# Kernel tuning notes

Measured on AMD Instinct MI355X. Metric: run time of the kernel, lower is better.

## Reference

```python
import jax, jax.numpy as jnp
import numpy as np
import math

B, S, D = 2, 2048, 1024
H, KV, HD = 16, 4, 64
G = H // KV          # kv groups
CAP = 50.0           # attention soft-cap
EPS = 1e-6           # RMSNorm eps


def _rmsnorm(x, w):
    return x * jax.lax.rsqrt(jnp.mean(x * x, axis=-1, keepdims=True) + EPS) * w


def _rope(x, freqs):
    # x: (b, h, s, hd); freqs: (S, hd//2, 2) with [...,0]=cos, [...,1]=sin
    s = x.shape[2]
    xp = x.reshape(*x.shape[:-1], -1, 2)
    cos = freqs[:s, :, 0][None, None]   # (1,1,s,hd//2)
    sin = freqs[:s, :, 1][None, None]
    x0, x1 = xp[..., 0], xp[..., 1]
    out = jnp.stack([x0 * cos - x1 * sin, x0 * sin + x1 * cos], axis=-1)
    return out.reshape(x.shape)


def setup_inputs() -> dict:
    key = jax.random.key(0)
    ks = jax.random.split(key, 6)
    x = jax.random.normal(ks[0], (B, S, D), dtype=jnp.float32)
    # realistic RoPE table: theta_i = pos / 10000^(2i/hd)
    inv_freq = 1.0 / (10000.0 ** (np.arange(0, HD, 2, dtype=np.float32) / HD))
    theta = np.arange(S, dtype=np.float32)[:, None] * inv_freq[None, :]
    rope_freqs = jnp.asarray(np.stack([np.cos(theta), np.sin(theta)], axis=-1))
    sc = 0.02
    wq = jax.random.normal(ks[1], (2 * H * HD, D), dtype=jnp.float32) * sc
    wk = jax.random.normal(ks[2], (2 * KV * HD, D), dtype=jnp.float32) * sc
    wv = jax.random.normal(ks[3], (KV * HD, D), dtype=jnp.float32) * sc
    wo = jax.random.normal(ks[4], (D, H * HD), dtype=jnp.float32) * sc
    q_norm_w = jnp.ones((HD,), dtype=jnp.float32)
    k_norm_w = jnp.ones((HD,), dtype=jnp.float32)
    diff_lambda = jnp.array([0.8], dtype=jnp.float32)
    return {"x": x, "rope_freqs": rope_freqs, "wq": wq, "wk": wk, "wv": wv,
            "wo": wo, "q_norm_w": q_norm_w, "k_norm_w": k_norm_w,
            "diff_lambda": diff_lambda}


def reference(x, rope_freqs, wq, wk, wv, wo, q_norm_w, k_norm_w, diff_lambda):
    b, s, _ = x.shape
    # projections (torch Linear: y = x @ W^T)
    q = (x @ wq.T).reshape(b, s, H, 2 * HD).transpose(0, 2, 1, 3)   # (b,H,s,2hd)
    k = (x @ wk.T).reshape(b, s, KV, 2 * HD).transpose(0, 2, 1, 3)  # (b,KV,s,2hd)
    v = (x @ wv.T).reshape(b, s, KV, HD).transpose(0, 2, 1, 3)      # (b,KV,s,hd)
    q1, q2 = jnp.split(q, 2, axis=-1)
    k1, k2 = jnp.split(k, 2, axis=-1)
    # QK-norm (before RoPE, as in the torch module)
    q1, q2 = _rmsnorm(q1, q_norm_w), _rmsnorm(q2, q_norm_w)
    k1, k2 = _rmsnorm(k1, k_norm_w), _rmsnorm(k2, k_norm_w)
    # RoPE
    q1, q2 = _rope(q1, rope_freqs), _rope(q2, rope_freqs)
    k1, k2 = _rope(k1, rope_freqs), _rope(k2, rope_freqs)
    # GQA expansion: each kv head repeated G times contiguously
    k1 = jnp.repeat(k1, G, axis=1)
    k2 = jnp.repeat(k2, G, axis=1)
    v = jnp.repeat(v, G, axis=1)
    scale = 1.0 / math.sqrt(HD)
    scores1 = jnp.einsum('bhqd,bhkd->bhqk', q1, k1) * scale
    scores2 = jnp.einsum('bhqd,bhkd->bhqk', q2, k2) * scale
    # soft-cap
    scores1 = CAP * jnp.tanh(scores1 / CAP)
    scores2 = CAP * jnp.tanh(scores2 / CAP)
    mask = jnp.triu(jnp.full((s, s), -jnp.inf, dtype=scores1.dtype), 1)
    attn1 = jax.nn.softmax(scores1 + mask, axis=-1)
    attn2 = jax.nn.softmax(scores2 + mask, axis=-1)
    diff_attn = attn1 - diff_lambda[0] * attn2
    out = jnp.einsum('bhqk,bhkd->bhqd', diff_attn, v)
    out = out.transpose(0, 2, 1, 3).reshape(b, s, H * HD)
    return out @ wo.T
```

## Files before the change

### kernel.cpp

```cpp
#include <hip/hip_runtime.h>
#include <hip/hip_bf16.h>

#define B_ 2
#define S_ 2048
#define D_ 1024
#define H_ 16
#define KV_ 4
#define HD_ 64
#define G_ (H_ / KV_)
#define NCAT 2816
#define VOFF 2560

typedef __attribute__((ext_vector_type(8))) short short8;
typedef __attribute__((ext_vector_type(4))) short short4v;
typedef __attribute__((ext_vector_type(2))) int int2v;
typedef __attribute__((ext_vector_type(4))) float floatx4;

using gvoid_p = const __attribute__((address_space(1))) void*;
using lvoid_p = __attribute__((address_space(3))) void*;

__device__ inline void gload_lds16(const short* g, short* l) {
    __builtin_amdgcn_global_load_lds((gvoid_p)(const void*)g, (lvoid_p)(void*)l, 16, 0, 0);
}

__device__ inline int cvt_pk_bf16(float lo, float hi) {
    int r;
    asm volatile("v_cvt_pk_bf16_f32 %0, %1, %2" : "=v"(r) : "v"(lo), "v"(hi));
    return r;
}

__global__ void cvt5_kernel(const float* s0, const float* s1, const float* s2,
                            const float* s3, const float* s4,
                            __hip_bfloat16* d0, __hip_bfloat16* d1, __hip_bfloat16* d2,
                            __hip_bfloat16* d3, __hip_bfloat16* d4,
                            int n0, int n1, int n2, int n3, int n4) {
    const float* s; __hip_bfloat16* d; int n;
    switch (blockIdx.y) {
        case 0: s = s0; d = d0; n = n0; break;
        case 1: s = s1; d = d1; n = n1; break;
        case 2: s = s2; d = d2; n = n2; break;
        case 3: s = s3; d = d3; n = n3; break;
        default: s = s4; d = d4; n = n4; break;
    }
    int nv = n >> 2;
    for (int i = blockIdx.x * blockDim.x + threadIdx.x; i < nv;
         i += gridDim.x * blockDim.x) {
        floatx4 v = ((const floatx4*)s)[i];
        short4v o;
#pragma unroll
        for (int e = 0; e < 4; ++e) {
            __hip_bfloat16 hh = __float2bfloat16(v[e]);
            o[e] = __builtin_bit_cast(short, hh);
        }
        ((short4v*)d)[i] = o;
    }
}

template <typename OutT>
__global__ __launch_bounds__(256) void gemm_bt_lds(const short* __restrict__ A,
                                                   const short* __restrict__ Bm,
                                                   OutT* __restrict__ C,
                                                   int M, int N, int K) {
    __shared__ __align__(16) short As[2][128 * 32];
    __shared__ __align__(16) short Bs[2][128 * 32];
    int tid = threadIdx.x;
    int wid = tid >> 6, lane = tid & 63;
    int wr = wid >> 1, wc = wid & 1;
    int r = lane & 15, kq = lane >> 4;

    int nwg = gridDim.x * gridDim.y;
    int orig = blockIdx.y * gridDim.x + blockIdx.x;
    int wg = (orig & 7) * (nwg >> 3) + (orig >> 3);
    int bx = wg % gridDim.x, by = wg / gridDim.x;

    long m0 = (long)by * 128;
    long n0 = (long)bx * 128;

    const short* gA0 = A + (m0 + (tid >> 2)) * (long)K + (tid & 3) * 8;
    const short* gA1 = A + (m0 + 64 + (tid >> 2)) * (long)K + (tid & 3) * 8;
    const short* gB0 = Bm + (n0 + (tid >> 2)) * (long)K + (tid & 3) * 8;
    const short* gB1 = Bm + (n0 + 64 + (tid >> 2)) * (long)K + (tid & 3) * 8;

    auto stage = [&](int buf, int k0) {
        gload_lds16(gA0 + k0, &As[buf][wid * 512]);
        gload_lds16(gA1 + k0, &As[buf][2048 + wid * 512]);
        gload_lds16(gB0 + k0, &Bs[buf][wid * 512]);
        gload_lds16(gB1 + k0, &Bs[buf][2048 + wid * 512]);
    };

    floatx4 acc[4][4];
#pragma unroll
    for (int i = 0; i < 4; ++i)
#pragma unroll
        for (int j = 0; j < 4; ++j) acc[i][j] = {0.f, 0.f, 0.f, 0.f};

    int nt = K >> 5;
    stage(0, 0);
    for (int t = 0; t < nt; ++t) {
        int cur = t & 1;
        __builtin_amdgcn_s_barrier();
        if (t + 1 < nt) {
            stage(cur ^ 1, (t + 1) << 5);
            asm volatile("s_waitcnt vmcnt(4)" ::: "memory");
        } else {
            asm volatile("s_waitcnt vmcnt(0)" ::: "memory");
        }
        __builtin_amdgcn_sched_barrier(0);
        __builtin_amdgcn_s_barrier();
        short8 a[4], b[4];
#pragma unroll
        for (int mi = 0; mi < 4; ++mi)
            a[mi] = *(const short8*)&As[cur][(wr * 64 + mi * 16 + r) * 32 + kq * 8];
#pragma unroll
        for (int ni = 0; ni < 4; ++ni)
            b[ni] = *(const short8*)&Bs[cur][(wc * 64 + ni * 16 + r) * 32 + kq * 8];
#pragma unroll
        for (int mi = 0; mi < 4; ++mi)
#pragma unroll
            for (int ni = 0; ni < 4; ++ni)
                acc[mi][ni] = __builtin_amdgcn_mfma_f32_16x16x32_bf16(
                    a[mi], b[ni], acc[mi][ni], 0, 0, 0);
    }
    int col_l = lane & 15, row_l = (lane >> 4) * 4;
#pragma unroll
    for (int mi = 0; mi < 4; ++mi)
#pragma unroll
        for (int ni = 0; ni < 4; ++ni) {
            long col = n0 + wc * 64 + ni * 16 + col_l;
            long row0 = m0 + wr * 64 + mi * 16 + row_l;
#pragma unroll
            for (int j = 0; j < 4; ++j) {
                float v = acc[mi][ni][j];
                if constexpr (__is_same(OutT, float))
                    C[(row0 + j) * N + col] = v;
                else
                    C[(row0 + j) * N + col] = __float2bfloat16(v);
            }
        }
}

__global__ void norm_rope_kernel(const __hip_bfloat16* __restrict__ buf,
                                 __hip_bfloat16* __restrict__ outb,
                                 const float* __restrict__ freqs,
                                 const float* __restrict__ w, int nvec, int nh,
                                 int tstride, int colbase) {
    int gt = blockIdx.x * blockDim.x + threadIdx.x;
    int gw = gt >> 6;
    int lane = gt & 63;
    if (gw >= nvec) return;
    int t = gw / (nh * 2);
    int rem = gw - t * (nh * 2);
    int s = t & (S_ - 1);
    const __hip_bfloat16* v = buf + (long)t * tstride + colbase + rem * 64;
    float x = __bfloat162float(v[lane]);
    float ss = x * x;
#pragma unroll
    for (int off = 32; off; off >>= 1) ss += __shfl_xor(ss, off);
    float r = rsqrtf(ss * (1.f / 64.f) + 1e-6f);
    x = x * r * w[lane];
    int i = lane >> 1;
    float c  = freqs[(s * (HD_ / 2) + i) * 2];
    float sn = freqs[(s * (HD_ / 2) + i) * 2 + 1];
    float p = __shfl_xor(x, 1);
    float y = (lane & 1) ? fmaf(p, sn, x * c) : fmaf(x, c, -(p * sn));
    outb[(long)gw * 64 + lane] = __float2bfloat16(y);
}

__global__ __launch_bounds__(256) void v_transpose_kernel(const short* __restrict__ src,
                                                          short* __restrict__ dst) {
    __shared__ short ls[64][72];
    int s0 = blockIdx.x * 64;
    int kv = blockIdx.y, b = blockIdx.z;
    int tid = threadIdx.x;
    const short* base = src + ((long)(b * S_ + s0)) * NCAT + VOFF + kv * 64;
    {
        int rr = tid >> 2, cc = (tid & 3) * 16;
        *(short8*)&ls[rr][cc]     = *(const short8*)(base + (long)rr * NCAT + cc);
        *(short8*)&ls[rr][cc + 8] = *(const short8*)(base + (long)rr * NCAT + cc + 8);
    }
    __syncthreads();
    short* ob = dst + ((long)(b * KV_ + kv) * 64) * S_ + s0;
    {
        int d = tid >> 2, sl = (tid & 3) * 16;
        short8 o0, o1;
#pragma unroll
        for (int e = 0; e < 8; ++e) { o0[e] = ls[sl + e][d]; o1[e] = ls[sl + 8 + e][d]; }
        *(short8*)(ob + (long)d * S_ + sl)     = o0;
        *(short8*)(ob + (long)d * S_ + sl + 8) = o1;
    }
}

__global__ __launch_bounds__(256, 4) void attn_kernel(const short* __restrict__ qb,
                                                      const short* __restrict__ kbuf,
                                                      const short* __restrict__ vtb,
                                                      __hip_bfloat16* __restrict__ ob,
                                                      float* __restrict__ part,
                                                      float* __restrict__ lpart,
                                                      const float* __restrict__ lam_p) {
    __shared__ __align__(16) short Ks[2][32][128];
    __shared__ __align__(16) short Vt[2][64][40];

    int tid = threadIdx.x, w = tid >> 6, lane = tid & 63;
    int b = blockIdx.z, h = blockIdx.y, kv = h / G_;
    int p = (int)blockIdx.x >> 1, e = (int)blockIdx.x & 1;
    int qtA = p, qtB = 31 - p;
    int r = lane & 15, kq = lane >> 4;
    float lam = lam_p[0];

    floatx4 acc[2][4];
    floatx4 accl[2];
    short8 qa[2][2];

    const short* vbase = vtb + (long)(b * KV_ + kv) * 64 * S_;
    const float c1 = 0.18033688f, nc4 = -3.7570e-7f, zoff = -17.3123405f;
    const short one_bf = (short)0x3F80;
    short4v ones4 = {one_bf, one_bf, one_bf, one_bf};

    int ch1 = tid + 256;
    int krow0 = tid >> 4, kcs0 = ((tid & 15) ^ (krow0 & 7)) * 8;
    int krow1 = ch1 >> 4, kcs1 = ((ch1 & 15) ^ (krow1 & 7)) * 8;
    const short* kgb = kbuf + ((long)b * S_ * KV_ + kv) * 128;
    int vd = tid >> 2, vch = tid & 3;

    auto issueK = [&](int buf, int ki) {
        long rb = (long)(ki * 32) * (KV_ * 128);
        gload_lds16(kgb + rb + (long)krow0 * (KV_ * 128) + kcs0, &Ks[buf][0][0] + w * 512);
        gload_lds16(kgb + rb + (long)krow1 * (KV_ * 128) + kcs1, &Ks[buf][0][0] + 2048 + w * 512);
    };
    auto loadV = [&](int kb) {
        return *(const short8*)(vbase + (long)vd * S_ + kb + vch * 8);
    };

    auto reset_acc = [&]() {
#pragma unroll
        for (int m = 0; m < 2; ++m) {
            accl[m] = {0.f, 0.f, 0.f, 0.f};
#pragma unroll
            for (int dt = 0; dt < 4; ++dt) acc[m][dt] = {0.f, 0.f, 0.f, 0.f};
        }
    };
    auto load_q = [&](int q0) {
        const short* qrow = qb + ((long)(b * S_ + q0 + r) * H_ + h) * 128;
        qa[0][0] = *(const short8*)(qrow + kq * 8);
        qa[0][1] = *(const short8*)(qrow + 32 + kq * 8);
        qa[1][0] = *(const short8*)(qrow + 64 + kq * 8);
        qa[1][1] = *(const short8*)(qrow + 96 + kq * 8);
    };

    auto tile_compute = [&](int cur, int kb, int q0, bool domask) {
        int rel = q0 + r - kb;
#pragma unroll
        for (int m = 0; m < 2; ++m) {
            floatx4 sacc[2];
#pragma unroll
            for (int nt = 0; nt < 2; ++nt) {
                sacc[nt] = {0.f, 0.f, 0.f, 0.f};
                const short* row = &Ks[cur][nt * 16 + r][0];
                short8 a0 = *(const short8*)(row + (((m * 8) + kq) ^ (r & 7)) * 8);
                short8 a1 = *(const short8*)(row + (((m * 8) + 4 + kq) ^ (r & 7)) * 8);
                sacc[nt] = __builtin_amdgcn_mfma_f32_16x16x32_bf16(a0, qa[m][0], sacc[nt], 0, 0, 0);
                sacc[nt] = __builtin_amdgcn_mfma_f32_16x16x32_bf16(a1, qa[m][1], sacc[nt], 0, 0, 0);
            }
            short4v pa[2];
#pragma unroll
            for (int nt = 0; nt < 2; ++nt) {
                float pv[4];
#pragma unroll
                for (int j = 0; j < 4; ++j) {
                    float raw = sacc[nt][j];
                    float r2 = raw * raw;
                    float z = fmaf(raw, fmaf(r2, nc4, c1), zoff);
                    pv[j] = __builtin_amdgcn_exp2f(z);
                    if (domask && (nt * 16 + kq * 4 + j > rel)) pv[j] = 0.f;
                }
                int lo = cvt_pk_bf16(pv[0], pv[1]);
                int hi = cvt_pk_bf16(pv[2], pv[3]);
                pa[nt] = __builtin_bit_cast(short4v, int2v{lo, hi});
            }
#pragma unroll
            for (int dt = 0; dt < 4; ++dt) {
#pragma unroll
                for (int nt = 0; nt < 2; ++nt) {
                    short4v vb = *(const short4v*)&Vt[cur][dt * 16 + r][nt * 16 + kq * 4];
                    acc[m][dt] = __builtin_amdgcn_mfma_f32_16x16x16bf16_1k(
                        pa[nt], vb, acc[m][dt], 0, 0, 0);
                }
            }
#pragma unroll
            for (int nt = 0; nt < 2; ++nt)
                accl[m] = __builtin_amdgcn_mfma_f32_16x16x16bf16_1k(
                    pa[nt], ones4, accl[m], 0, 0, 0);
        }
    };

    auto run = [&](int qt, int ki0, int ki1, bool diag) {
        int q0 = qt * 64 + w * 16;
        load_q(q0);
        reset_acc();
        int nseg = ki1 - ki0;
        issueK(0, ki0);
        short8 rva = loadV(ki0 * 32), rvb;
        for (int ii = 0; ii < nseg; ++ii) {
            int ki = ki0 + ii, cur = ii & 1;
            bool pre = (ii + 1 < nseg);
            if (pre) issueK(cur ^ 1, ki + 1);
            if (pre) asm volatile("s_waitcnt vmcnt(2)" ::: "memory");
            else     asm volatile("s_waitcnt vmcnt(0)" ::: "memory");
            __builtin_amdgcn_sched_barrier(0);
            if (cur == 0) {
                *(short8*)&Vt[0][vd][vch * 8] = rva;
                if (pre) rvb = loadV((ki + 1) * 32);
            } else {
                *(short8*)&Vt[1][vd][vch * 8] = rvb;
                if (pre) rva = loadV((ki + 1) * 32);
            }
            asm volatile("s_waitcnt lgkmcnt(0)" ::: "memory");
            __builtin_amdgcn_sched_barrier(0);
            __builtin_amdgcn_s_barrier();
            tile_compute(cur, ki * 32, q0, diag && ((ki >> 1) == qt));
        }
        __builtin_amdgcn_s_barrier();
    };

    if (e == 0) {
        run(qtA, 0, 2 * qtA + 2, true);
        {
            int q0 = qtA * 64 + w * 16;
#pragma unroll
            for (int j = 0; j < 4; ++j) {
                float i1 = 1.f / accl[0][j];
                float i2 = lam / accl[1][j];
                int qr = q0 + kq * 4 + j;
                __hip_bfloat16* orow = ob + ((long)(b * S_ + qr) * H_ + h) * 64;
#pragma unroll
                for (int dt = 0; dt < 4; ++dt) {
                    float val = acc[0][dt][j] * i1 - acc[1][dt][j] * i2;
                    orow[dt * 16 + r] = __float2bfloat16(val);
                }
            }
        }
        run(qtB, 0, 31 - 2 * p, false);
    } else {
        run(qtB, 31 - 2 * p, 64 - 2 * p, true);
    }

    {
        long slot = (long)(b * H_ + h) * 16 + (qtB - 16);
        long base = ((slot * 2 + e) * 2) * 4096L;
        int qloc = w * 16 + kq * 4;
#pragma unroll
        for (int m = 0; m < 2; ++m)
#pragma unroll
            for (int dt = 0; dt < 4; ++dt)
#pragma unroll
                for (int j = 0; j < 4; ++j)
                    part[base + m * 4096L + (qloc + j) * 64 + dt * 16 + r] = acc[m][dt][j];
        if (r == 0) {
#pragma unroll
            for (int m = 0; m < 2; ++m)
#pragma unroll
                for (int j = 0; j < 4; ++j)
                    lpart[((slot * 2 + e) * 2 + m) * 64 + qloc + j] = accl[m][j];
        }
    }
}

__global__ __launch_bounds__(256) void attn_merge_kernel(const float* __restrict__ part,
                                                         const float* __restrict__ lpart,
                                                         __hip_bfloat16* __restrict__ ob,
                                                         const float* __restrict__ lam_p) {
    long sid = blockIdx.x;
    int t16 = sid & 15;
    int h = (sid >> 4) & (H_ - 1);
    int b = (int)(sid >> 8);
    int qt = 16 + t16;
    float lam = lam_p[0];
    const float* p0 = part + sid * 4 * 4096L;
    const float* p1 = part + (sid * 4 + 2) * 4096L;
    const float* l0 = lpart + sid * 4 * 64L;
    const float* l1 = lpart + (sid * 4 + 2) * 64L;
    int tid = threadIdx.x;
#pragma unroll
    for (int i = 0; i < 16; ++i) {
        int idx = i * 256 + tid;
        int q = idx >> 6, d = idx & 63;
        float a1 = p0[q * 64 + d] + p1[q * 64 + d];
        float a2 = p0[4096 + q * 64 + d] + p1[4096 + q * 64 + d];
        float L1 = l0[q] + l1[q];
        float L2 = l0[64 + q] + l1[64 + q];
        float val = a1 / L1 - lam * (a2 / L2);
        ob[((long)(b * S_ + qt * 64 + q) * H_ + h) * 64 + d] = __float2bfloat16(val);
    }
}

extern "C" void kernel_launch(void* const* d_in, const int* in_sizes, int n_in,
                              void* d_out, int out_size, void* d_ws, size_t ws_size,
                              hipStream_t stream) {
    const float* x     = (const float*)d_in[0];
    const float* freqs = (const float*)d_in[1];
    const float* wq    = (const float*)d_in[2];
    const float* wk    = (const float*)d_in[3];
    const float* wv    = (const float*)d_in[4];
    const float* wo    = (const float*)d_in[5];
    const float* qnw   = (const float*)d_in[6];
    const float* knw   = (const float*)d_in[7];
    const float* lam   = (const float*)d_in[8];
    float* out = (float*)d_out;

    const int T = B_ * S_;
    char* ws = (char*)d_ws;
    size_t off = 0;
    auto alloc = [&](size_t bytes) {
        void* p = ws + off;
        off += (bytes + 255) & ~(size_t)255;
        return p;
    };
    __hip_bfloat16* xb   = (__hip_bfloat16*)alloc((size_t)T * D_ * 2);
    __hip_bfloat16* wcat = (__hip_bfloat16*)alloc((size_t)NCAT * D_ * 2);
    __hip_bfloat16* wob  = (__hip_bfloat16*)alloc((size_t)D_ * D_ * 2);
    __hip_bfloat16* qkvb = (__hip_bfloat16*)alloc((size_t)T * NCAT * 2);
    __hip_bfloat16* qb16 = (__hip_bfloat16*)alloc((size_t)T * 2 * H_ * HD_ * 2);
    __hip_bfloat16* kb16 = (__hip_bfloat16*)alloc((size_t)T * 2 * KV_ * HD_ * 2);
    __hip_bfloat16* vT   = (__hip_bfloat16*)alloc((size_t)B_ * KV_ * HD_ * S_ * 2);
    float* part  = (float*)alloc((size_t)512 * 2 * 2 * 4096 * 4);
    float* lpart = (float*)alloc((size_t)512 * 2 * 2 * 64 * 4);
    __hip_bfloat16* aob  = xb;

    cvt5_kernel<<<dim3(2048, 5), 256, 0, stream>>>(
        x, wq, wk, wv, wo,
        xb, wcat, wcat + (size_t)2 * H_ * HD_ * D_,
        wcat + (size_t)(2 * H_ * HD_ + 2 * KV_ * HD_) * D_, wob,
        T * D_, 2 * H_ * HD_ * D_, 2 * KV_ * HD_ * D_, KV_ * HD_ * D_, D_ * D_);

    gemm_bt_lds<__hip_bfloat16><<<dim3(NCAT / 128, T / 128), 256, 0, stream>>>(
        (const short*)xb, (const short*)wcat, qkvb, T, NCAT, D_);

    {
        int nvq = T * H_ * 2;
        norm_rope_kernel<<<(nvq * 64 + 255) / 256, 256, 0, stream>>>(
            qkvb, qb16, freqs, qnw, nvq, H_, NCAT, 0);
        int nvk = T * KV_ * 2;
        norm_rope_kernel<<<(nvk * 64 + 255) / 256, 256, 0, stream>>>(
            qkvb, kb16, freqs, knw, nvk, KV_, NCAT, 2 * H_ * HD_);
        v_transpose_kernel<<<dim3(S_ / 64, KV_, B_), 256, 0, stream>>>(
            (const short*)qkvb, (short*)vT);
    }

    attn_kernel<<<dim3(32, H_, B_), 256, 0, stream>>>(
        (const short*)qb16, (const short*)kb16, (const short*)vT, aob, part, lpart, lam);
    attn_merge_kernel<<<512, 256, 0, stream>>>(part, lpart, aob, lam);

    gemm_bt_lds<float><<<dim3(D_ / 128, T / 128), 256, 0, stream>>>(
        (const short*)aob, (const short*)wob, out, T, D_, D_);
}
```

Measured before the change: 174.1 us.

## Use 16x16x32 MFMA for PV, preload V fragments, triple-buffer K tiles

The P·V product and the row-sum accumulation now use 16x16x32 bf16 MFMAs. Both key sub-tiles are packed into one short8 operand, which halves the number of PV and row-sum MFMA instructions. V fragments are loaded from LDS once per tile, before the two head-half loops, instead of inside each loop. K shared memory goes from two buffers to three, rotating so the prefetch writes a buffer that no lagging wave can still be reading. The extra buffer raises LDS use per block, which could reduce occupancy, and the PV operand layout has to stay consistent with the k-index mapping of the larger MFMA.

```diff
diff --git a/kernel.cpp b/kernel.cpp
--- a/kernel.cpp
+++ b/kernel.cpp
@@ -14,6 +14,7 @@
 typedef __attribute__((ext_vector_type(8))) short short8;
 typedef __attribute__((ext_vector_type(4))) short short4v;
 typedef __attribute__((ext_vector_type(2))) int int2v;
+typedef __attribute__((ext_vector_type(4))) int int4v;
 typedef __attribute__((ext_vector_type(4))) float floatx4;
 
 using gvoid_p = const __attribute__((address_space(1))) void*;
@@ -197,7 +198,7 @@
                                                       float* __restrict__ part,
                                                       float* __restrict__ lpart,
                                                       const float* __restrict__ lam_p) {
-    __shared__ __align__(16) short Ks[2][32][128];
+    __shared__ __align__(16) short Ks[3][32][128];
     __shared__ __align__(16) short Vt[2][64][40];
 
     int tid = threadIdx.x, w = tid >> 6, lane = tid & 63;
@@ -214,7 +215,7 @@
     const short* vbase = vtb + (long)(b * KV_ + kv) * 64 * S_;
     const float c1 = 0.18033688f, nc4 = -3.7570e-7f, zoff = -17.3123405f;
     const short one_bf = (short)0x3F80;
-    short4v ones4 = {one_bf, one_bf, one_bf, one_bf};
+    short8 ones8 = {one_bf, one_bf, one_bf, one_bf, one_bf, one_bf, one_bf, one_bf};
 
     int ch1 = tid + 256;
     int krow0 = tid >> 4, kcs0 = ((tid & 15) ^ (krow0 & 7)) * 8;
@@ -247,49 +248,55 @@
         qa[1][1] = *(const short8*)(qrow + 96 + kq * 8);
     };
 
-    auto tile_compute = [&](int cur, int kb, int q0, bool domask) {
+    auto tile_compute = [&](int bk, int cv, int kb, int q0, bool domask) {
         int rel = q0 + r - kb;
+        short8 vb[4];
+#pragma unroll
+        for (int dt = 0; dt < 4; ++dt) {
+            const short* vrow = &Vt[cv][dt * 16 + r][0];
+            int2v lo = *(const int2v*)(vrow + 4 * kq);
+            int2v hi = *(const int2v*)(vrow + 16 + 4 * kq);
+            vb[dt] = __builtin_bit_cast(short8, int4v{lo[0], lo[1], hi[0], hi[1]});
+        }
 #pragma unroll
         for (int m = 0; m < 2; ++m) {
             floatx4 sacc[2];
 #pragma unroll
             for (int nt = 0; nt < 2; ++nt) {
                 sacc[nt] = {0.f, 0.f, 0.f, 0.f};
-                const short* row = &Ks[cur][nt * 16 + r][0];
+                const short* row = &Ks[bk][nt * 16 + r][0];
                 short8 a0 = *(const short8*)(row + (((m * 8) + kq) ^ (r & 7)) * 8);
                 short8 a1 = *(const short8*)(row + (((m * 8) + 4 + kq) ^ (r & 7)) * 8);
                 sacc[nt] = __builtin_amdgcn_mfma_f32_16x16x32_bf16(a0, qa[m][0], sacc[nt], 0, 0, 0);
                 sacc[nt] = __builtin_amdgcn_mfma_f32_16x16x32_bf16(a1, qa[m][1], sacc[nt], 0, 0, 0);
             }
-            short4v pa[2];
-#pragma unroll
-            for (int nt = 0; nt < 2; ++nt) {
-                float pv[4];
+            float pv[2][4];
+#pragma unroll
+            for (int nt = 0; nt < 2; ++nt)
 #pragma unroll
                 for (int j = 0; j < 4; ++j) {
                     float raw = sacc[nt][j];
                     float r2 = raw * raw;
                     float z = fmaf(raw, fmaf(r2, nc4, c1), zoff);
-                    pv[j] = __builtin_amdgcn_exp2f(z);
-                    if (domask && (nt * 16 + kq * 4 + j > rel)) pv[j] = 0.f;
+                    pv[nt][j] = __builtin_amdgcn_exp2f(z);
                 }
-                int lo = cvt_pk_bf16(pv[0], pv[1]);
-                int hi = cvt_pk_bf16(pv[2], pv[3]);
-                pa[nt] = __builtin_bit_cast(short4v, int2v{lo, hi});
+            if (domask) {
+#pragma unroll
+                for (int nt = 0; nt < 2; ++nt)
+#pragma unroll
+                    for (int j = 0; j < 4; ++j)
+                        if (nt * 16 + kq * 4 + j > rel) pv[nt][j] = 0.f;
             }
-#pragma unroll
-            for (int dt = 0; dt < 4; ++dt) {
-#pragma unroll
-                for (int nt = 0; nt < 2; ++nt) {
-                    short4v vb = *(const short4v*)&Vt[cur][dt * 16 + r][nt * 16 + kq * 4];
-                    acc[m][dt] = __builtin_amdgcn_mfma_f32_16x16x16bf16_1k(
-                        pa[nt], vb, acc[m][dt], 0, 0, 0);
-                }
-            }
-#pragma unroll
-            for (int nt = 0; nt < 2; ++nt)
-                accl[m] = __builtin_amdgcn_mfma_f32_16x16x16bf16_1k(
-                    pa[nt], ones4, accl[m], 0, 0, 0);
+            int d0 = cvt_pk_bf16(pv[0][0], pv[0][1]);
+            int d1 = cvt_pk_bf16(pv[0][2], pv[0][3]);
+            int d2 = cvt_pk_bf16(pv[1][0], pv[1][1]);
+            int d3 = cvt_pk_bf16(pv[1][2], pv[1][3]);
+            short8 pa8 = __builtin_bit_cast(short8, int4v{d0, d1, d2, d3});
+#pragma unroll
+            for (int dt = 0; dt < 4; ++dt)
+                acc[m][dt] = __builtin_amdgcn_mfma_f32_16x16x32_bf16(
+                    pa8, vb[dt], acc[m][dt], 0, 0, 0);
+            accl[m] = __builtin_amdgcn_mfma_f32_16x16x32_bf16(pa8, ones8, accl[m], 0, 0, 0);
         }
     };
 
@@ -300,14 +307,16 @@
         int nseg = ki1 - ki0;
         issueK(0, ki0);
         short8 rva = loadV(ki0 * 32), rvb;
+        int bk = 0;
         for (int ii = 0; ii < nseg; ++ii) {
-            int ki = ki0 + ii, cur = ii & 1;
+            int ki = ki0 + ii, cv = ii & 1;
             bool pre = (ii + 1 < nseg);
-            if (pre) issueK(cur ^ 1, ki + 1);
+            int bk1 = (bk == 2) ? 0 : bk + 1;
+            if (pre) issueK(bk1, ki + 1);
             if (pre) asm volatile("s_waitcnt vmcnt(2)" ::: "memory");
             else     asm volatile("s_waitcnt vmcnt(0)" ::: "memory");
             __builtin_amdgcn_sched_barrier(0);
-            if (cur == 0) {
+            if (cv == 0) {
                 *(short8*)&Vt[0][vd][vch * 8] = rva;
                 if (pre) rvb = loadV((ki + 1) * 32);
             } else {
@@ -317,7 +326,8 @@
             asm volatile("s_waitcnt lgkmcnt(0)" ::: "memory");
             __builtin_amdgcn_sched_barrier(0);
             __builtin_amdgcn_s_barrier();
-            tile_compute(cur, ki * 32, q0, diag && ((ki >> 1) == qt));
+            tile_compute(bk, cv, ki * 32, q0, diag && ((ki >> 1) == qt));
+            bk = bk1;
         }
         __builtin_amdgcn_s_barrier();
     };
```

After: 174.6 us. Within noise of the previous version (+0.3%).
